# Kernel tuning notes

Hardware: AMD Instinct MI355X
Metric: run time of the kernel (lower is better)

The kernel has to match this reference:

```python
import jax, jax.numpy as jnp
import numpy as np

N_NODES = 10000
N_EDGES = 160000
BATCH = 32
IN_FEAT = 64
POLY_K = 5
OUT_FEAT = 128


def setup_inputs() -> dict:
    key = jax.random.key(0)
    k_x, k_r, k_c, k_v, k_w, k_b = jax.random.split(key, 6)
    x = jax.random.normal(k_x, (BATCH, N_NODES, IN_FEAT), dtype=jnp.float32)
    lap_rows = jax.random.randint(k_r, (N_EDGES,), 0, N_NODES, dtype=jnp.int32)
    lap_cols = jax.random.randint(k_c, (N_EDGES,), 0, N_NODES, dtype=jnp.int32)
    # small values keep the degree-5 Chebyshev recurrence numerically tame
    lap_vals = jax.random.normal(k_v, (N_EDGES,), dtype=jnp.float32) * 0.05
    weight = jax.random.normal(k_w, (IN_FEAT * POLY_K, OUT_FEAT), dtype=jnp.float32) * 0.1
    bias = jax.random.normal(k_b, (1, 1, OUT_FEAT), dtype=jnp.float32) * 0.1
    return {"x": x, "lap_rows": lap_rows, "lap_cols": lap_cols,
            "lap_vals": lap_vals, "weight": weight, "bias": bias,
            "pooling_size": 4}


def _spmm(rows, cols, vals, m):
    # sparse [N,N] @ dense [N,M] via gather + segment_sum
    return jax.ops.segment_sum(vals[:, None] * m[cols], rows, num_segments=N_NODES)


def reference(x, lap_rows, lap_cols, lap_vals, weight, bias, pooling_size):
    B, N, F = x.shape
    K = POLY_K
    Fo = weight.shape[1]
    # x0: [N, F*B]
    x0 = jnp.transpose(x, (1, 2, 0)).reshape(N, F * B)
    terms = [x0]
    if K > 1:
        x1 = _spmm(lap_rows, lap_cols, lap_vals, x0)
        terms.append(x1)
        for _ in range(2, K):
            x2 = 2.0 * _spmm(lap_rows, lap_cols, lap_vals, x1) - x0
            terms.append(x2)
            x0, x1 = x1, x2
    xk = jnp.stack(terms, axis=0)                      # [K, N, F*B]
    xk = xk.reshape(K, N, F, B)
    xk = jnp.transpose(xk, (3, 1, 2, 0))               # [B, N, F, K]
    xk = xk.reshape(B * N, F * K)
    out = (xk @ weight).reshape(B, N, Fo)              # dense projection
    out = jax.nn.relu(out + bias)                      # bias + ReLU
    if pooling_size > 1:
        out = out.reshape(B, N // pooling_size, pooling_size, Fo).max(axis=2)
    return out
```

## Files before the change

kernel.cpp:

```cpp
#include <hip/hip_runtime.h>
#include <hip/hip_bf16.h>
#include <cstddef>
#include <cstdint>

#define N_NODES 10000
#define N_EDGES 160000
#define BATCH 32
#define IN_FEAT 64
#define POLY_K 5
#define OUT_FEAT 128
#define KTOT 320
#define POOLSZ 4
#define NPOOL 2500
#define NSL 16

typedef short bf16x8 __attribute__((ext_vector_type(8)));
typedef unsigned short u16x8 __attribute__((ext_vector_type(8)));
typedef unsigned int u32x4 __attribute__((ext_vector_type(4)));
typedef float f32x4 __attribute__((ext_vector_type(4)));
typedef float f32x2 __attribute__((ext_vector_type(2)));

__device__ __forceinline__ unsigned short f2bf(float f) {
  unsigned int u = __float_as_uint(f);
  unsigned int r = u + 0x7FFFu + ((u >> 16) & 1u);
  return (unsigned short)(r >> 16);
}
__device__ __forceinline__ float bf2f(unsigned short u) {
  return __uint_as_float(((unsigned int)u) << 16);
}
__device__ __forceinline__ f32x2 unpk(unsigned int u) {
  f32x2 r;
  r[0] = __uint_as_float(u << 16);
  r[1] = __uint_as_float(u & 0xFFFF0000u);
  return r;
}


__global__ void zero_int_kernel(int* __restrict__ p, int n) {
  int i = blockIdx.x * 256 + threadIdx.x;
  if (i < n) p[i] = 0;
}

__global__ void hist_kernel(const int* __restrict__ rows, int* __restrict__ deg) {
  int e = blockIdx.x * 256 + threadIdx.x;
  if (e < N_EDGES) atomicAdd(&deg[rows[e]], 1);
}

__global__ void scan_kernel(const int* __restrict__ deg, int* __restrict__ row_start,
                            int* __restrict__ cursor) {
  __shared__ int wsum[16];
  __shared__ int carry_sm;
  int t = threadIdx.x;
  int lane = t & 63, wid = t >> 6;
  if (t == 0) { carry_sm = 0; row_start[0] = 0; }
  __syncthreads();
  for (int base = 0; base < N_NODES; base += 1024) {
    int idx = base + t;
    int v = (idx < N_NODES) ? deg[idx] : 0;
    int x = v;
    #pragma unroll
    for (int off = 1; off < 64; off <<= 1) {
      int y = __shfl_up(x, off, 64);
      if (lane >= off) x += y;
    }
    if (lane == 63) wsum[wid] = x;
    __syncthreads();
    if (wid == 0) {
      int sv = (lane < 16) ? wsum[lane] : 0;
      #pragma unroll
      for (int off = 1; off < 16; off <<= 1) {
        int y = __shfl_up(sv, off, 64);
        if (lane >= off) sv += y;
      }
      if (lane < 16) wsum[lane] = sv;
    }
    __syncthreads();
    int incl = x + (wid > 0 ? wsum[wid - 1] : 0) + carry_sm;
    if (idx < N_NODES) {
      row_start[idx + 1] = incl;
      cursor[idx] = incl - v;
    }
    __syncthreads();
    if (t == 1023) carry_sm = incl;
    __syncthreads();
  }
}

__global__ void scatter_kernel(const int* __restrict__ rows, const int* __restrict__ cols,
                               const float* __restrict__ vals, int* __restrict__ cursor,
                               int2* __restrict__ csr_pairs) {
  int e = blockIdx.x * 256 + threadIdx.x;
  if (e < N_EDGES) {
    int r = rows[e];
    int p = atomicAdd(&cursor[r], 1);
    csr_pairs[p] = make_int2(cols[e], __float_as_int(vals[e]));
  }
}


__global__ void bsort_kernel(const int* __restrict__ deg, int* __restrict__ perm) {
  int chunk = blockIdx.x * 256 + threadIdx.x;
  if (chunk >= (N_NODES + 15) / 16) return;
  int base = chunk * 16;
  int idx[16], dg[16];
  #pragma unroll
  for (int j = 0; j < 16; ++j) {
    int r = base + j;
    idx[j] = r;
    dg[j] = (r < N_NODES) ? deg[r] : 0x7fffffff;
  }
  #pragma unroll
  for (int a = 1; a < 16; ++a) {
    int dv = dg[a], iv = idx[a];
    int b = a - 1;
    while (b >= 0 && dg[b] > dv) { dg[b + 1] = dg[b]; idx[b + 1] = idx[b]; --b; }
    dg[b + 1] = dv; idx[b + 1] = iv;
  }
  #pragma unroll
  for (int j = 0; j < 16; ++j)
    if (base + j < N_NODES) perm[base + j] = idx[j];
}


__global__ void wpack_kernel(const float* __restrict__ weight, unsigned short* __restrict__ wpack) {
  int id = blockIdx.x * 256 + threadIdx.x;
  if (id >= 5120) return;
  int ft = id / 640;
  int c = (id / 64) % 10;
  int l = id % 64;
  int fo = ft * 16 + (l & 15);
  unsigned short v[8];
  #pragma unroll
  for (int j = 0; j < 8; ++j) {
    int k = c * 32 + ((l >> 4)) * 8 + j;
    int row = (k & 63) * POLY_K + (k >> 6);
    v[j] = f2bf(weight[row * OUT_FEAT + fo]);
  }
  ushort4* dst = (ushort4*)&wpack[(size_t)id * 8];
  dst[0] = make_ushort4(v[0], v[1], v[2], v[3]);
  dst[1] = make_ushort4(v[4], v[5], v[6], v[7]);
}


template <int BB>
__global__ __launch_bounds__(256) void transpose_kernel(const float* __restrict__ x,
                                                        unsigned short* __restrict__ t0, int b0) {
  constexpr int CB = 64 * BB;
  constexpr int SCOLS = CB / NSL;
  constexpr size_t SLICE_SL = (size_t)N_NODES * SCOLS;
  constexpr int NN = 8;
  int n0 = blockIdx.x * NN;
  int t = threadIdx.x;
  int bsub = t >> 6;
  int n = (t >> 3) & 7;
  int f8 = t & 7;
  int node = n0 + n;
  #pragma unroll
  for (int bi = 0; bi < BB / 4; ++bi) {
    int b = bi * 4 + bsub;
    const float* xp = &x[((size_t)(b0 + b) * N_NODES + node) * IN_FEAT + f8 * 8];
    float4 v0 = *(const float4*)xp;
    float4 v1 = *(const float4*)(xp + 4);
    u16x8 o;
    o[0] = f2bf(v0.x); o[1] = f2bf(v0.y); o[2] = f2bf(v0.z); o[3] = f2bf(v0.w);
    o[4] = f2bf(v1.x); o[5] = f2bf(v1.y); o[6] = f2bf(v1.z); o[7] = f2bf(v1.w);
    int i = b * 64 + f8 * 8;
    int sl = i / SCOLS;
    int cw = i - sl * SCOLS;
    *(u16x8*)&t0[(size_t)sl * SLICE_SL + (size_t)node * SCOLS + cw] = o;
  }
}


template <int BB>
__global__ __launch_bounds__(256) void spmm_kernel(const unsigned short* __restrict__ xin,
                                                   const unsigned short* __restrict__ prev,
                                                   unsigned short* __restrict__ xout,
                                                   const int* __restrict__ row_start,
                                                   const int2* __restrict__ csr_pairs,
                                                   const int* __restrict__ perm,
                                                   float alpha, int use_prev) {
  constexpr int CB = 64 * BB;
  constexpr int SCOLS = CB / NSL;
  constexpr size_t SLICE_SL = (size_t)N_NODES * SCOLS;
  constexpr int LPR = SCOLS / 8;
  constexpr int RPB = 256 / LPR;
  constexpr int RB = (N_NODES + RPB - 1) / RPB;
  constexpr int PHB = RB * 8;
  int bid = blockIdx.x;
  int phase = bid / PHB;
  int rem = bid - phase * PHB;
  int xcd = rem & 7;
  int rowblk = rem >> 3;
  int slice = phase * 8 + xcd;
  int t = threadIdx.x;
  int rl = t / LPR;
  int cl = t - rl * LPR;
  int si = rowblk * RPB + rl;
  if (si >= N_NODES) return;
  int n = perm[si];
  unsigned off = (unsigned)cl * 8u;

  const unsigned short* xs = xin  + (size_t)slice * SLICE_SL;
  const unsigned short* ps = prev + (size_t)slice * SLICE_SL;
  unsigned short*       os = xout + (size_t)slice * SLICE_SL;

  int s = row_start[n];
  int e = row_start[n + 1];
  f32x2 a0 = {0.f, 0.f}, a1 = {0.f, 0.f}, a2 = {0.f, 0.f}, a3 = {0.f, 0.f};

  int i = s;
  for (; i + 7 < e; i += 8) {
    int2 E[8];
    #pragma unroll
    for (int u = 0; u < 8; ++u) E[u] = csr_pairs[i + u];
    u32x4 d[8];
    #pragma unroll
    for (int u = 0; u < 8; ++u) d[u] = *(const u32x4*)&xs[(unsigned)E[u].x * SCOLS + off];
    #pragma unroll
    for (int u = 0; u < 8; ++u) {
      float vv = __int_as_float(E[u].y);
      f32x2 w = {vv, vv};
      a0 = __builtin_elementwise_fma(w, unpk(d[u][0]), a0);
      a1 = __builtin_elementwise_fma(w, unpk(d[u][1]), a1);
      a2 = __builtin_elementwise_fma(w, unpk(d[u][2]), a2);
      a3 = __builtin_elementwise_fma(w, unpk(d[u][3]), a3);
    }
  }
  for (; i + 3 < e; i += 4) {
    int2 E[4];
    #pragma unroll
    for (int u = 0; u < 4; ++u) E[u] = csr_pairs[i + u];
    u32x4 d[4];
    #pragma unroll
    for (int u = 0; u < 4; ++u) d[u] = *(const u32x4*)&xs[(unsigned)E[u].x * SCOLS + off];
    #pragma unroll
    for (int u = 0; u < 4; ++u) {
      float vv = __int_as_float(E[u].y);
      f32x2 w = {vv, vv};
      a0 = __builtin_elementwise_fma(w, unpk(d[u][0]), a0);
      a1 = __builtin_elementwise_fma(w, unpk(d[u][1]), a1);
      a2 = __builtin_elementwise_fma(w, unpk(d[u][2]), a2);
      a3 = __builtin_elementwise_fma(w, unpk(d[u][3]), a3);
    }
  }
  for (; i < e; ++i) {
    int2 E0 = csr_pairs[i];
    u32x4 d0 = *(const u32x4*)&xs[(unsigned)E0.x * SCOLS + off];
    float vv = __int_as_float(E0.y);
    f32x2 w0 = {vv, vv};
    a0 = __builtin_elementwise_fma(w0, unpk(d0[0]), a0);
    a1 = __builtin_elementwise_fma(w0, unpk(d0[1]), a1);
    a2 = __builtin_elementwise_fma(w0, unpk(d0[2]), a2);
    a3 = __builtin_elementwise_fma(w0, unpk(d0[3]), a3);
  }

  unsigned nelt = (unsigned)n * SCOLS + off;
  u16x8 o;
  if (use_prev) {
    u32x4 qd = *(const u32x4*)&ps[nelt];
    f32x2 q0 = unpk(qd[0]), q1 = unpk(qd[1]), q2 = unpk(qd[2]), q3 = unpk(qd[3]);
    o[0] = f2bf(alpha * a0[0] - q0[0]); o[1] = f2bf(alpha * a0[1] - q0[1]);
    o[2] = f2bf(alpha * a1[0] - q1[0]); o[3] = f2bf(alpha * a1[1] - q1[1]);
    o[4] = f2bf(alpha * a2[0] - q2[0]); o[5] = f2bf(alpha * a2[1] - q2[1]);
    o[6] = f2bf(alpha * a3[0] - q3[0]); o[7] = f2bf(alpha * a3[1] - q3[1]);
  } else {
    o[0] = f2bf(alpha * a0[0]); o[1] = f2bf(alpha * a0[1]);
    o[2] = f2bf(alpha * a1[0]); o[3] = f2bf(alpha * a1[1]);
    o[4] = f2bf(alpha * a2[0]); o[5] = f2bf(alpha * a2[1]);
    o[6] = f2bf(alpha * a3[0]); o[7] = f2bf(alpha * a3[1]);
  }
  *(u16x8*)&os[nelt] = o;
}


template <int BB>
__global__ __launch_bounds__(256, 4) void gemm_mfma_kernel(const unsigned short* __restrict__ slices,
                                                           const unsigned short* __restrict__ wpack,
                                                           const float* __restrict__ bias,
                                                           float* __restrict__ out, int b0) {
  constexpr int CB = 64 * BB;
  constexpr int SCOLS = CB / NSL;
  constexpr size_t SLICE_SL = (size_t)N_NODES * SCOLS;
  constexpr int MB = (BB >= 16) ? 16 : BB;
  constexpr int MT = MB / 4;
  constexpr int SPAN = MB * 64;
  constexpr int ROWS = 4 * MB;
  constexpr int CHUNKS = ROWS * 40;
  __shared__ unsigned short A[POLY_K * ROWS * 64];

  int g = blockIdx.x;
  int bh = blockIdx.y;
  int t = threadIdx.x;

  auto stage = [&](int idx0) {
    int idx = idx0 + t;
    int kpoly = idx / (ROWS * 8);
    int rem = idx - kpoly * (ROWS * 8);
    int row = rem >> 3;
    int cphys = idx & 7;
    int clog3 = cphys ^ (row & 7);
    int fb = clog3 * 8;
    int bloc = row >> 2;
    int nd = row & 3;
    int c = bh * SPAN + bloc * 64 + fb;
    int sl = c / SCOLS;
    int cw = c & (SCOLS - 1);
    const unsigned short* gsrc = &slices[((size_t)kpoly * NSL + sl) * SLICE_SL +
                                         (size_t)(g * POOLSZ + nd) * SCOLS + cw];
    unsigned short* lbase = &A[(size_t)(idx0 + (t & 192)) * 8];
    __builtin_amdgcn_global_load_lds((const __attribute__((address_space(1))) unsigned int*)gsrc,
                                     (__attribute__((address_space(3))) unsigned int*)lbase,
                                     16, 0, 0);
  };

  int w = t >> 6;
  int l = t & 63;
  int lm = l & 15;
  int q = l >> 4;
  int swz = lm & 7;

  f32x4 acc[MT][2];
  #pragma unroll
  for (int mt = 0; mt < MT; ++mt)
    #pragma unroll
    for (int fj = 0; fj < 2; ++fj) {
      acc[mt][fj][0] = 0.f; acc[mt][fj][1] = 0.f;
      acc[mt][fj][2] = 0.f; acc[mt][fj][3] = 0.f;
    }

  if constexpr (MB == 16) {
    constexpr int PH1 = 2 * ROWS * 8;
    for (int idx0 = 0; idx0 < PH1; idx0 += 256) stage(idx0);
    bf16x8 bpre[4][2];
    #pragma unroll
    for (int c = 0; c < 4; ++c)
      #pragma unroll
      for (int fj = 0; fj < 2; ++fj)
        bpre[c][fj] = *(const bf16x8*)&wpack[(size_t)((((w * 2 + fj) * 10) + c) * 64 + l) * 8];
    __syncthreads();
    for (int idx0 = PH1; idx0 < CHUNKS; idx0 += 256) stage(idx0);
    #pragma unroll
    for (int c = 0; c < 4; ++c) {
      #pragma unroll
      for (int mt = 0; mt < MT; ++mt) {
        bf16x8 afrag = *(const bf16x8*)
            &A[((c >> 1) * ROWS + mt * 16 + lm) * 64 + ((((c & 1) * 4 + q) ^ swz) << 3)];
        acc[mt][0] = __builtin_amdgcn_mfma_f32_16x16x32_bf16(afrag, bpre[c][0], acc[mt][0], 0, 0, 0);
        acc[mt][1] = __builtin_amdgcn_mfma_f32_16x16x32_bf16(afrag, bpre[c][1], acc[mt][1], 0, 0, 0);
      }
    }
    __syncthreads();
    #pragma unroll
    for (int c = 4; c < 10; ++c) {
      bf16x8 bfrag[2];
      #pragma unroll
      for (int fj = 0; fj < 2; ++fj)
        bfrag[fj] = *(const bf16x8*)&wpack[(size_t)((((w * 2 + fj) * 10) + c) * 64 + l) * 8];
      #pragma unroll
      for (int mt = 0; mt < MT; ++mt) {
        bf16x8 afrag = *(const bf16x8*)
            &A[((c >> 1) * ROWS + mt * 16 + lm) * 64 + ((((c & 1) * 4 + q) ^ swz) << 3)];
        acc[mt][0] = __builtin_amdgcn_mfma_f32_16x16x32_bf16(afrag, bfrag[0], acc[mt][0], 0, 0, 0);
        acc[mt][1] = __builtin_amdgcn_mfma_f32_16x16x32_bf16(afrag, bfrag[1], acc[mt][1], 0, 0, 0);
      }
    }
  } else {
    for (int idx0 = 0; idx0 < CHUNKS; idx0 += 256) stage(idx0);
    __syncthreads();
    #pragma unroll
    for (int c = 0; c < 10; ++c) {
      bf16x8 bfrag[2];
      #pragma unroll
      for (int fj = 0; fj < 2; ++fj)
        bfrag[fj] = *(const bf16x8*)&wpack[(size_t)((((w * 2 + fj) * 10) + c) * 64 + l) * 8];
      #pragma unroll
      for (int mt = 0; mt < MT; ++mt) {
        bf16x8 afrag = *(const bf16x8*)
            &A[((c >> 1) * ROWS + mt * 16 + lm) * 64 + ((((c & 1) * 4 + q) ^ swz) << 3)];
        acc[mt][0] = __builtin_amdgcn_mfma_f32_16x16x32_bf16(afrag, bfrag[0], acc[mt][0], 0, 0, 0);
        acc[mt][1] = __builtin_amdgcn_mfma_f32_16x16x32_bf16(afrag, bfrag[1], acc[mt][1], 0, 0, 0);
      }
    }
  }

  #pragma unroll
  for (int fj = 0; fj < 2; ++fj) {
    int fo = (w * 2 + fj) * 16 + lm;
    float bv = bias[fo];
    #pragma unroll
    for (int mt = 0; mt < MT; ++mt) {
      float mx = fmaxf(fmaxf(acc[mt][fj][0], acc[mt][fj][1]),
                       fmaxf(acc[mt][fj][2], acc[mt][fj][3]));
      float val = fmaxf(mx + bv, 0.f);
      int b = b0 + bh * MB + mt * 4 + q;
      out[((size_t)b * NPOOL + g) * OUT_FEAT + fo] = val;
    }
  }
}


template <int BB>
static void run_pipeline(const float* x, const float* bias,
                         const int* row_start, const int2* csr_pairs, const int* perm,
                         const unsigned short* wpack,
                         unsigned short* slices, float* out, hipStream_t stream) {
  constexpr int CB = 64 * BB;
  constexpr size_t TERM = (size_t)N_NODES * CB;
  constexpr int LPR = (CB / NSL) / 8;
  constexpr int RPB = 256 / LPR;
  constexpr int NBLK = ((N_NODES + RPB - 1) / RPB) * NSL;
  constexpr int MB = (BB >= 16) ? 16 : BB;
  for (int b0 = 0; b0 < BATCH; b0 += BB) {
    transpose_kernel<BB><<<N_NODES / 8, 256, 0, stream>>>(x, slices, b0);
    for (int k = 1; k < POLY_K; ++k) {
      const unsigned short* xin  = slices + (size_t)(k - 1) * TERM;
      const unsigned short* prev = (k >= 2) ? slices + (size_t)(k - 2) * TERM : slices;
      unsigned short* xout = slices + (size_t)k * TERM;
      float alpha = (k == 1) ? 1.0f : 2.0f;
      spmm_kernel<BB><<<NBLK, 256, 0, stream>>>(xin, prev, xout, row_start,
                                                csr_pairs, perm, alpha,
                                                (k >= 2) ? 1 : 0);
    }
    gemm_mfma_kernel<BB><<<dim3(NPOOL, BB / MB), 256, 0, stream>>>(slices, wpack, bias, out, b0);
  }
}

static size_t needed_bytes(int BB) {
  return 1522176u + (size_t)6400000 * BB;
}

extern "C" void kernel_launch(void* const* d_in, const int* in_sizes, int n_in,
                              void* d_out, int out_size, void* d_ws, size_t ws_size,
                              hipStream_t stream) {
  const float* x        = (const float*)d_in[0];
  const int*   lap_rows = (const int*)d_in[1];
  const int*   lap_cols = (const int*)d_in[2];
  const float* lap_vals = (const float*)d_in[3];
  const float* weight   = (const float*)d_in[4];
  const float* bias     = (const float*)d_in[5];
  float* out = (float*)d_out;

  int* deg       = (int*)d_ws;
  int* cursor    = deg + 10016;
  int* row_start = cursor + 10016;
  int* perm      = row_start + 10016;
  int2* csr_pairs = (int2*)(perm + 10016);
  unsigned short* wpack = (unsigned short*)(csr_pairs + N_EDGES);
  unsigned short* slices = wpack + 40960;

  int BB = 0;
  if      (ws_size >= needed_bytes(32)) BB = 32;
  else if (ws_size >= needed_bytes(16)) BB = 16;
  else if (ws_size >= needed_bytes(8))  BB = 8;
  else if (ws_size >= needed_bytes(4))  BB = 4;
  if (BB == 0) return;

  zero_int_kernel<<<(N_NODES + 255) / 256, 256, 0, stream>>>(deg, N_NODES);
  hist_kernel<<<(N_EDGES + 255) / 256, 256, 0, stream>>>(lap_rows, deg);
  scan_kernel<<<1, 1024, 0, stream>>>(deg, row_start, cursor);
  scatter_kernel<<<(N_EDGES + 255) / 256, 256, 0, stream>>>(lap_rows, lap_cols, lap_vals,
                                                            cursor, csr_pairs);
  bsort_kernel<<<3, 256, 0, stream>>>(deg, perm);
  wpack_kernel<<<20, 256, 0, stream>>>(weight, wpack);

  switch (BB) {
    case 32: run_pipeline<32>(x, bias, row_start, csr_pairs, perm, wpack, slices, out, stream); break;
    case 16: run_pipeline<16>(x, bias, row_start, csr_pairs, perm, wpack, slices, out, stream); break;
    case 8:  run_pipeline<8>(x, bias, row_start, csr_pairs, perm, wpack, slices, out, stream); break;
    case 4:  run_pipeline<4>(x, bias, row_start, csr_pairs, perm, wpack, slices, out, stream); break;
  }
}
```

Measured before the change: 417.1 us.

## Map one wavefront per SpMM row with 4-byte lanes and drop degree sort

The SpMM thread mapping changes from each lane owning 8 bf16 columns (16-byte gathers) to each lane owning 2 columns (4-byte gathers). With BB=32 a whole 64-lane wavefront now covers one row, so row bounds become wave-uniform via readfirstlane and there is no intra-wave divergence from differing degrees. The degree-bucket sort kernel and the perm indirection are removed because divergence no longer needs balancing. The cost is four times as many threads and narrower per-lane memory accesses, plus redundant per-lane CSR loads, which may cut effective gather bandwidth.

```diff
diff --git a/kernel.cpp b/kernel.cpp
--- a/kernel.cpp
+++ b/kernel.cpp
@@ -95,30 +95,6 @@
     int p = atomicAdd(&cursor[r], 1);
     csr_pairs[p] = make_int2(cols[e], __float_as_int(vals[e]));
   }
-}
-
-
-__global__ void bsort_kernel(const int* __restrict__ deg, int* __restrict__ perm) {
-  int chunk = blockIdx.x * 256 + threadIdx.x;
-  if (chunk >= (N_NODES + 15) / 16) return;
-  int base = chunk * 16;
-  int idx[16], dg[16];
-  #pragma unroll
-  for (int j = 0; j < 16; ++j) {
-    int r = base + j;
-    idx[j] = r;
-    dg[j] = (r < N_NODES) ? deg[r] : 0x7fffffff;
-  }
-  #pragma unroll
-  for (int a = 1; a < 16; ++a) {
-    int dv = dg[a], iv = idx[a];
-    int b = a - 1;
-    while (b >= 0 && dg[b] > dv) { dg[b + 1] = dg[b]; idx[b + 1] = idx[b]; --b; }
-    dg[b + 1] = dv; idx[b + 1] = iv;
-  }
-  #pragma unroll
-  for (int j = 0; j < 16; ++j)
-    if (base + j < N_NODES) perm[base + j] = idx[j];
 }
 
 
@@ -178,13 +154,13 @@
                                                    unsigned short* __restrict__ xout,
                                                    const int* __restrict__ row_start,
                                                    const int2* __restrict__ csr_pairs,
-                                                   const int* __restrict__ perm,
                                                    float alpha, int use_prev) {
   constexpr int CB = 64 * BB;
   constexpr int SCOLS = CB / NSL;
   constexpr size_t SLICE_SL = (size_t)N_NODES * SCOLS;
-  constexpr int LPR = SCOLS / 8;
-  constexpr int RPB = 256 / LPR;
+  constexpr int LPR = SCOLS / 2;
+  constexpr int RPW = 64 / LPR;
+  constexpr int RPB = 4 * RPW;
   constexpr int RB = (N_NODES + RPB - 1) / RPB;
   constexpr int PHB = RB * 8;
   int bid = blockIdx.x;
@@ -194,12 +170,13 @@
   int rowblk = rem >> 3;
   int slice = phase * 8 + xcd;
   int t = threadIdx.x;
-  int rl = t / LPR;
-  int cl = t - rl * LPR;
-  int si = rowblk * RPB + rl;
-  if (si >= N_NODES) return;
-  int n = perm[si];
-  unsigned off = (unsigned)cl * 8u;
+  int wid = t >> 6;
+  int lane = t & 63;
+  int rw = lane / LPR;
+  int cl = lane - rw * LPR;
+  int n = rowblk * RPB + wid * RPW + rw;
+  if (n >= N_NODES) return;
+  unsigned off = (unsigned)cl * 2u;
 
   const unsigned short* xs = xin  + (size_t)slice * SLICE_SL;
   const unsigned short* ps = prev + (size_t)slice * SLICE_SL;
@@ -207,70 +184,48 @@
 
   int s = row_start[n];
   int e = row_start[n + 1];
-  f32x2 a0 = {0.f, 0.f}, a1 = {0.f, 0.f}, a2 = {0.f, 0.f}, a3 = {0.f, 0.f};
+  if constexpr (RPW == 1) {
+    s = __builtin_amdgcn_readfirstlane(s);
+    e = __builtin_amdgcn_readfirstlane(e);
+  }
+  f32x2 a = {0.f, 0.f};
 
   int i = s;
   for (; i + 7 < e; i += 8) {
     int2 E[8];
     #pragma unroll
     for (int u = 0; u < 8; ++u) E[u] = csr_pairs[i + u];
-    u32x4 d[8];
-    #pragma unroll
-    for (int u = 0; u < 8; ++u) d[u] = *(const u32x4*)&xs[(unsigned)E[u].x * SCOLS + off];
+    unsigned d[8];
+    #pragma unroll
+    for (int u = 0; u < 8; ++u) d[u] = *(const unsigned*)&xs[(unsigned)E[u].x * SCOLS + off];
     #pragma unroll
     for (int u = 0; u < 8; ++u) {
       float vv = __int_as_float(E[u].y);
       f32x2 w = {vv, vv};
-      a0 = __builtin_elementwise_fma(w, unpk(d[u][0]), a0);
-      a1 = __builtin_elementwise_fma(w, unpk(d[u][1]), a1);
-      a2 = __builtin_elementwise_fma(w, unpk(d[u][2]), a2);
-      a3 = __builtin_elementwise_fma(w, unpk(d[u][3]), a3);
-    }
-  }
-  for (; i + 3 < e; i += 4) {
-    int2 E[4];
-    #pragma unroll
-    for (int u = 0; u < 4; ++u) E[u] = csr_pairs[i + u];
-    u32x4 d[4];
-    #pragma unroll
-    for (int u = 0; u < 4; ++u) d[u] = *(const u32x4*)&xs[(unsigned)E[u].x * SCOLS + off];
-    #pragma unroll
-    for (int u = 0; u < 4; ++u) {
-      float vv = __int_as_float(E[u].y);
-      f32x2 w = {vv, vv};
-      a0 = __builtin_elementwise_fma(w, unpk(d[u][0]), a0);
-      a1 = __builtin_elementwise_fma(w, unpk(d[u][1]), a1);
-      a2 = __builtin_elementwise_fma(w, unpk(d[u][2]), a2);
-      a3 = __builtin_elementwise_fma(w, unpk(d[u][3]), a3);
+      a = __builtin_elementwise_fma(w, unpk(d[u]), a);
     }
   }
   for (; i < e; ++i) {
     int2 E0 = csr_pairs[i];
-    u32x4 d0 = *(const u32x4*)&xs[(unsigned)E0.x * SCOLS + off];
+    unsigned d0 = *(const unsigned*)&xs[(unsigned)E0.x * SCOLS + off];
     float vv = __int_as_float(E0.y);
     f32x2 w0 = {vv, vv};
-    a0 = __builtin_elementwise_fma(w0, unpk(d0[0]), a0);
-    a1 = __builtin_elementwise_fma(w0, unpk(d0[1]), a1);
-    a2 = __builtin_elementwise_fma(w0, unpk(d0[2]), a2);
-    a3 = __builtin_elementwise_fma(w0, unpk(d0[3]), a3);
+    a = __builtin_elementwise_fma(w0, unpk(d0), a);
   }
 
   unsigned nelt = (unsigned)n * SCOLS + off;
-  u16x8 o;
+  float v0, v1;
   if (use_prev) {
-    u32x4 qd = *(const u32x4*)&ps[nelt];
-    f32x2 q0 = unpk(qd[0]), q1 = unpk(qd[1]), q2 = unpk(qd[2]), q3 = unpk(qd[3]);
-    o[0] = f2bf(alpha * a0[0] - q0[0]); o[1] = f2bf(alpha * a0[1] - q0[1]);
-    o[2] = f2bf(alpha * a1[0] - q1[0]); o[3] = f2bf(alpha * a1[1] - q1[1]);
-    o[4] = f2bf(alpha * a2[0] - q2[0]); o[5] = f2bf(alpha * a2[1] - q2[1]);
-    o[6] = f2bf(alpha * a3[0] - q3[0]); o[7] = f2bf(alpha * a3[1] - q3[1]);
+    unsigned qd = *(const unsigned*)&ps[nelt];
+    f32x2 q = unpk(qd);
+    v0 = alpha * a[0] - q[0];
+    v1 = alpha * a[1] - q[1];
   } else {
-    o[0] = f2bf(alpha * a0[0]); o[1] = f2bf(alpha * a0[1]);
-    o[2] = f2bf(alpha * a1[0]); o[3] = f2bf(alpha * a1[1]);
-    o[4] = f2bf(alpha * a2[0]); o[5] = f2bf(alpha * a2[1]);
-    o[6] = f2bf(alpha * a3[0]); o[7] = f2bf(alpha * a3[1]);
-  }
-  *(u16x8*)&os[nelt] = o;
+    v0 = alpha * a[0];
+    v1 = alpha * a[1];
+  }
+  unsigned outw = (unsigned)f2bf(v0) | ((unsigned)f2bf(v1) << 16);
+  *(unsigned*)&os[nelt] = outw;
 }
 
 
@@ -402,13 +357,15 @@
 
 template <int BB>
 static void run_pipeline(const float* x, const float* bias,
-                         const int* row_start, const int2* csr_pairs, const int* perm,
+                         const int* row_start, const int2* csr_pairs,
                          const unsigned short* wpack,
                          unsigned short* slices, float* out, hipStream_t stream) {
   constexpr int CB = 64 * BB;
   constexpr size_t TERM = (size_t)N_NODES * CB;
-  constexpr int LPR = (CB / NSL) / 8;
-  constexpr int RPB = 256 / LPR;
+  constexpr int SCOLS = CB / NSL;
+  constexpr int LPR = SCOLS / 2;
+  constexpr int RPW = 64 / LPR;
+  constexpr int RPB = 4 * RPW;
   constexpr int NBLK = ((N_NODES + RPB - 1) / RPB) * NSL;
   constexpr int MB = (BB >= 16) ? 16 : BB;
   for (int b0 = 0; b0 < BATCH; b0 += BB) {
@@ -419,7 +376,7 @@
       unsigned short* xout = slices + (size_t)k * TERM;
       float alpha = (k == 1) ? 1.0f : 2.0f;
       spmm_kernel<BB><<<NBLK, 256, 0, stream>>>(xin, prev, xout, row_start,
-                                                csr_pairs, perm, alpha,
+                                                csr_pairs, alpha,
                                                 (k >= 2) ? 1 : 0);
     }
     gemm_mfma_kernel<BB><<<dim3(NPOOL, BB / MB), 256, 0, stream>>>(slices, wpack, bias, out, b0);
@@ -444,8 +401,8 @@
   int* deg       = (int*)d_ws;
   int* cursor    = deg + 10016;
   int* row_start = cursor + 10016;
-  int* perm      = row_start + 10016;
-  int2* csr_pairs = (int2*)(perm + 10016);
+  int* spare     = row_start + 10016;
+  int2* csr_pairs = (int2*)(spare + 10016);
   unsigned short* wpack = (unsigned short*)(csr_pairs + N_EDGES);
   unsigned short* slices = wpack + 40960;
 
@@ -461,13 +418,12 @@
   scan_kernel<<<1, 1024, 0, stream>>>(deg, row_start, cursor);
   scatter_kernel<<<(N_EDGES + 255) / 256, 256, 0, stream>>>(lap_rows, lap_cols, lap_vals,
                                                             cursor, csr_pairs);
-  bsort_kernel<<<3, 256, 0, stream>>>(deg, perm);
   wpack_kernel<<<20, 256, 0, stream>>>(weight, wpack);
 
   switch (BB) {
-    case 32: run_pipeline<32>(x, bias, row_start, csr_pairs, perm, wpack, slices, out, stream); break;
-    case 16: run_pipeline<16>(x, bias, row_start, csr_pairs, perm, wpack, slices, out, stream); break;
-    case 8:  run_pipeline<8>(x, bias, row_start, csr_pairs, perm, wpack, slices, out, stream); break;
-    case 4:  run_pipeline<4>(x, bias, row_start, csr_pairs, perm, wpack, slices, out, stream); break;
-  }
-}
+    case 32: run_pipeline<32>(x, bias, row_start, csr_pairs, wpack, slices, out, stream); break;
+    case 16: run_pipeline<16>(x, bias, row_start, csr_pairs, wpack, slices, out, stream); break;
+    case 8:  run_pipeline<8>(x, bias, row_start, csr_pairs, wpack, slices, out, stream); break;
+    case 4:  run_pipeline<4>(x, bias, row_start, csr_pairs, wpack, slices, out, stream); break;
+  }
+}
```

New measurement: 484.6 us. 1.16x slower.
